# Performance work log

Hardware: AMD Instinct MI355X
Metric: run time of the kernel (lower is better)

The kernel has to match this reference:

```python
import jax, jax.numpy as jnp
import numpy as np

SEQ, B, D_IN, D_H = 512, 64, 512, 512


def setup_inputs() -> dict:
    key = jax.random.key(0)
    ks = jax.random.split(key, 5)
    s = 1.0 / np.sqrt(D_IN + D_H)
    inp = {
        "inputs": jax.random.normal(ks[0], (SEQ, B, D_IN), dtype=jnp.float32),
        "W_f": jax.random.normal(ks[1], (D_H, D_IN + D_H), dtype=jnp.float32) * s,
        "b_f": jnp.zeros((D_H,), jnp.float32),
        "W_i": jax.random.normal(ks[2], (D_H, D_IN + D_H), dtype=jnp.float32) * s,
        "b_i": jnp.zeros((D_H,), jnp.float32),
        "W_g": jax.random.normal(ks[3], (D_H, D_IN + D_H), dtype=jnp.float32) * s,
        "b_g": jnp.zeros((D_H,), jnp.float32),
        "W_o": jax.random.normal(ks[4], (D_H, D_IN + D_H), dtype=jnp.float32) * s,
        "b_o": jnp.zeros((D_H,), jnp.float32),
    }
    return inp


def reference(inputs, W_f, b_f, W_i, b_i, W_g, b_g, W_o, b_o):
    # inputs: [seq, batch, d_in]; states start at zeros (module default)
    B_ = inputs.shape[1]
    h0 = jnp.zeros((B_, D_H), inputs.dtype)
    c0 = jnp.zeros((B_, D_H), inputs.dtype)

    def step(carry, x_t):
        hx, cx = carry
        combined = jnp.concatenate([x_t, hx], axis=1)  # [B, d_in+d_h]
        f = jax.nn.sigmoid(combined @ W_f.T + b_f)
        i = jax.nn.sigmoid(combined @ W_i.T + b_i)
        g = jnp.tanh(combined @ W_g.T + b_g)
        o = jax.nn.sigmoid(combined @ W_o.T + b_o)
        cx = f * cx + i * g
        hx = o * jnp.tanh(cx)
        return (hx, cx), hx

    (hx, cx), stacked = jax.lax.scan(step, (h0, c0), inputs)
    return stacked, hx, cx
```

## Files before the change

kernel.cpp:

```cpp
#include <hip/hip_runtime.h>

#define SEQ   512
#define BATCH 64
#define DIN   512
#define DH    512
#define KTOT  1024
#define NWG   128
#define NTH   256
#define HBUF_BYTES 65536

#define FLAGS_BYTES 65536
#define HBASE_OFF   65536
#define XBF_OFF     (HBASE_OFF + 512 * HBUF_BYTES)
#define XBF_BYTES   ((size_t)SEQ * 4 * 16 * 1024)
#define WS_MODE1    ((size_t)HBASE_OFF + 511 * HBUF_BYTES)
#define WS_MODE2    ((size_t)XBF_OFF + XBF_BYTES)
#define FLAG_STRIDE 32

typedef __attribute__((ext_vector_type(8))) short short8;
typedef __attribute__((ext_vector_type(4))) float f32x4;

__device__ __forceinline__ float tanh_fast(float v) {
    const float e = __expf(2.0f * v);
    return 1.0f - 2.0f / (e + 1.0f);
}

__device__ __forceinline__ unsigned int f2bf(float f) {
    unsigned int u = __float_as_uint(f);
    return (u + 0x7fffu + ((u >> 16) & 1u)) >> 16;
}

__device__ __forceinline__ short8 cvt8(float4 lo, float4 hi) {
    short8 r;
    r[0] = (short)f2bf(lo.x); r[1] = (short)f2bf(lo.y);
    r[2] = (short)f2bf(lo.z); r[3] = (short)f2bf(lo.w);
    r[4] = (short)f2bf(hi.x); r[5] = (short)f2bf(hi.y);
    r[6] = (short)f2bf(hi.z); r[7] = (short)f2bf(hi.w);
    return r;
}

__device__ __forceinline__ unsigned int ld_flag(const unsigned int* p) {
    return __hip_atomic_load(p, __ATOMIC_RELAXED, __HIP_MEMORY_SCOPE_AGENT);
}
__device__ __forceinline__ void st_flag(unsigned int* p, unsigned int v) {
    __hip_atomic_store(p, v, __ATOMIC_RELAXED, __HIP_MEMORY_SCOPE_AGENT);
}
__device__ __forceinline__ unsigned long long ld_h_sc1(const unsigned long long* p) {
    return __hip_atomic_load(p, __ATOMIC_RELAXED, __HIP_MEMORY_SCOPE_AGENT);
}
__device__ __forceinline__ void st_h(unsigned long long* p, unsigned long long v) {
    __hip_atomic_store(p, v, __ATOMIC_RELAXED, __HIP_MEMORY_SCOPE_AGENT);
}

__global__ __launch_bounds__(256)
void xconv(const float* __restrict__ x, unsigned short* __restrict__ xbf)
{
    const int gid = blockIdx.x * 256 + threadIdx.x;
    const int l   = gid & 63;
    const int kt  = (gid >> 6) & 15;
    const int mtt = (gid >> 10) & 3;
    const int t   = gid >> 12;
    const float* src = x + ((size_t)t * BATCH + mtt * 16 + (l & 15)) * DIN
                         + kt * 32 + (l >> 4) * 8;
    *(short8*)(xbf + (size_t)gid * 8) =
        cvt8(*(const float4*)src, *(const float4*)(src + 4));
}

template <int MODE>
__global__ __launch_bounds__(NTH, 1)
void lstm_mfma(const float* __restrict__ x,
               const unsigned short* __restrict__ xbf,
               const float* __restrict__ Wf, const float* __restrict__ bfp,
               const float* __restrict__ Wi, const float* __restrict__ bip,
               const float* __restrict__ Wg, const float* __restrict__ bgp,
               const float* __restrict__ Wo, const float* __restrict__ bop,
               float* __restrict__ out,
               unsigned int* __restrict__ ws_u32)
{
    const int tid = threadIdx.x;
    const int l   = tid & 63;
    const int mt  = tid >> 6;
    const int wg  = blockIdx.x;
    const int j0  = wg * 4;

    const int n    = l & 15;
    const int khi  = l >> 4;
    const bool isg = (khi == 2);

    unsigned int* const flags = ws_u32;
    char* const hbase = (char*)ws_u32 + HBASE_OFF;

    const float* Wn = (n < 8) ? ((n < 4) ? Wf : Wi) : ((n < 12) ? Wg : Wo);
    const float* wrow = Wn + (size_t)(j0 + (n & 3)) * KTOT + khi * 8;
    short8 Bfr[32];
    #pragma unroll
    for (int kt = 0; kt < 32; ++kt) {
        Bfr[kt] = cvt8(*(const float4*)(wrow + kt * 32),
                       *(const float4*)(wrow + kt * 32 + 4));
    }
    const float* bptr = (khi == 0) ? bfp : (khi == 1) ? bip : (khi == 2) ? bgp : bop;
    const float4 bias4 = *(const float4*)(bptr + j0);

    float cst0 = 0.f, cst1 = 0.f, cst2 = 0.f, cst3 = 0.f;

    float* const hx_out = out + (size_t)SEQ * BATCH * DH;
    float* const cx_out = hx_out + (size_t)BATCH * DH;

    const int kth         = wg >> 3;
    const int lane_f_base = ((wg & 7) >> 1) << 4;
    const int half8       = (wg & 1) * 8;

    const unsigned int* const f0p = flags + ((size_t)mt * 128 + l) * FLAG_STRIDE;
    const unsigned int* const f1p = f0p + (size_t)64 * FLAG_STRIDE;
    unsigned int* const my_flag = flags + ((size_t)mt * 128 + wg) * FLAG_STRIDE;

    const float*  xrow_base = x + (size_t)(mt * 16 + (l & 15)) * DIN + khi * 8;
    const short8* xbf_base  = (const short8*)xbf + (size_t)mt * 16 * 64 + l;

    for (int t = 0; t < SEQ; ++t) {
        f32x4 acc_a = {0.f, 0.f, 0.f, 0.f};
        f32x4 acc_b = {0.f, 0.f, 0.f, 0.f};

        if (MODE == 2) {
            const short8* xp = xbf_base + (size_t)t * 4096;
            #pragma unroll
            for (int kt = 0; kt < 16; kt += 2) {
                acc_a = __builtin_amdgcn_mfma_f32_16x16x32_bf16(Bfr[kt], xp[kt * 64],
                                                                acc_a, 0, 0, 0);
                acc_b = __builtin_amdgcn_mfma_f32_16x16x32_bf16(Bfr[kt + 1], xp[(kt + 1) * 64],
                                                                acc_b, 0, 0, 0);
            }
        } else {
            const float* xr = xrow_base + (size_t)t * BATCH * DIN;
            #pragma unroll
            for (int kt = 0; kt < 16; kt += 2) {
                const short8 a0 = cvt8(*(const float4*)(xr + kt * 32),
                                       *(const float4*)(xr + kt * 32 + 4));
                const short8 a1 = cvt8(*(const float4*)(xr + (kt + 1) * 32),
                                       *(const float4*)(xr + (kt + 1) * 32 + 4));
                acc_a = __builtin_amdgcn_mfma_f32_16x16x32_bf16(Bfr[kt], a0, acc_a, 0, 0, 0);
                acc_b = __builtin_amdgcn_mfma_f32_16x16x32_bf16(Bfr[kt + 1], a1, acc_b, 0, 0, 0);
            }
        }

        if (t > 0) {
            const unsigned int target = (unsigned int)t;
            for (;;) {
                const unsigned int fa = ld_flag(f0p);
                const unsigned int fb = ld_flag(f1p);
                if (__all(fa >= target && fb >= target)) break;
                __builtin_amdgcn_s_sleep(1);
            }
            asm volatile("" ::: "memory");

            if (MODE == 0) {
                const unsigned long long* hp =
                    (const unsigned long long*)(hbase + ((t & 1) ^ 1) * HBUF_BYTES)
                    + ((size_t)(mt * 16) * 64 + l) * 2;
                #pragma unroll
                for (int kt = 0; kt < 16; kt += 2) {
                    union { unsigned long long u[2]; short8 v; } U0, U1;
                    U0.u[0] = ld_h_sc1(hp + kt * 128);
                    U0.u[1] = ld_h_sc1(hp + kt * 128 + 1);
                    U1.u[0] = ld_h_sc1(hp + (kt + 1) * 128);
                    U1.u[1] = ld_h_sc1(hp + (kt + 1) * 128 + 1);
                    acc_a = __builtin_amdgcn_mfma_f32_16x16x32_bf16(Bfr[16 + kt], U0.v,
                                                                    acc_a, 0, 0, 0);
                    acc_b = __builtin_amdgcn_mfma_f32_16x16x32_bf16(Bfr[17 + kt], U1.v,
                                                                    acc_b, 0, 0, 0);
                }
            } else {
                const uint4* hp = (const uint4*)(hbase + (size_t)(t - 1) * HBUF_BYTES)
                                  + ((size_t)(mt * 16) * 64 + l);
                uint4 hv[16];
                #pragma unroll
                for (int kt = 0; kt < 16; ++kt) hv[kt] = hp[kt * 64];
                #pragma unroll
                for (int kt = 0; kt < 16; kt += 2) {
                    union { uint4 u; short8 v; } U0, U1;
                    U0.u = hv[kt]; U1.u = hv[kt + 1];
                    acc_a = __builtin_amdgcn_mfma_f32_16x16x32_bf16(Bfr[16 + kt], U0.v,
                                                                    acc_a, 0, 0, 0);
                    acc_b = __builtin_amdgcn_mfma_f32_16x16x32_bf16(Bfr[17 + kt], U1.v,
                                                                    acc_b, 0, 0, 0);
                }
            }
        }

        float aq0, aq1, aq2, aq3;
        {
            const float m = isg ? 2.0f : 1.0f;
            const float p0 = acc_a[0] + acc_b[0] + bias4.x;
            const float p1 = acc_a[1] + acc_b[1] + bias4.y;
            const float p2 = acc_a[2] + acc_b[2] + bias4.z;
            const float p3 = acc_a[3] + acc_b[3] + bias4.w;
            const float y0 = 1.0f / (1.0f + __expf(-m * p0));
            const float y1 = 1.0f / (1.0f + __expf(-m * p1));
            const float y2 = 1.0f / (1.0f + __expf(-m * p2));
            const float y3 = 1.0f / (1.0f + __expf(-m * p3));
            aq0 = isg ? 2.0f * y0 - 1.0f : y0;
            aq1 = isg ? 2.0f * y1 - 1.0f : y1;
            aq2 = isg ? 2.0f * y2 - 1.0f : y2;
            aq3 = isg ? 2.0f * y3 - 1.0f : y3;
        }
        const float i0 = __shfl_xor(aq0, 16), g0 = __shfl_xor(aq0, 32), o0 = __shfl_xor(aq0, 48);
        const float i1 = __shfl_xor(aq1, 16), g1 = __shfl_xor(aq1, 32), o1 = __shfl_xor(aq1, 48);
        const float i2 = __shfl_xor(aq2, 16), g2 = __shfl_xor(aq2, 32), o2 = __shfl_xor(aq2, 48);
        const float i3 = __shfl_xor(aq3, 16), g3 = __shfl_xor(aq3, 32), o3 = __shfl_xor(aq3, 48);

        const bool active = (l < 16);
        float hq0 = 0.f, hq1 = 0.f, hq2 = 0.f, hq3 = 0.f;

        if (active) {
            cst0 = fmaf(aq0, cst0, i0 * g0); hq0 = o0 * tanh_fast(cst0);
            cst1 = fmaf(aq1, cst1, i1 * g1); hq1 = o1 * tanh_fast(cst1);
            cst2 = fmaf(aq2, cst2, i2 * g2); hq2 = o2 * tanh_fast(cst2);
            cst3 = fmaf(aq3, cst3, i3 * g3); hq3 = o3 * tanh_fast(cst3);

            if (t < SEQ - 1) {
                const unsigned long long pk =
                    (unsigned long long)(f2bf(hq0) | (f2bf(hq1) << 16))
                    | ((unsigned long long)(f2bf(hq2) | (f2bf(hq3) << 16)) << 32);
                char* const wb = (MODE == 0) ? hbase + (t & 1) * HBUF_BYTES
                                             : hbase + (size_t)t * HBUF_BYTES;
                unsigned long long* hp_w = (unsigned long long*)
                    (wb + (((size_t)(mt * 16 + kth) * 64
                            + (lane_f_base | l)) << 4) + half8);
                st_h(hp_w, pk);
            }
        }

        if (t < SEQ - 1) {
            asm volatile("s_waitcnt vmcnt(0)" ::: "memory");
            if (l == 0) st_flag(my_flag, (unsigned int)(t + 1));
        }

        if (active) {
            const int b = mt * 16 + l;
            const float4 ov = make_float4(hq0, hq1, hq2, hq3);
            *(float4*)(out + ((size_t)t * BATCH + b) * DH + j0) = ov;
            if (t == SEQ - 1) {
                *(float4*)(hx_out + (size_t)b * DH + j0) = ov;
                *(float4*)(cx_out + (size_t)b * DH + j0) =
                    make_float4(cst0, cst1, cst2, cst3);
            }
        }
    }
}

extern "C" void kernel_launch(void* const* d_in, const int* in_sizes, int n_in,
                              void* d_out, int out_size, void* d_ws, size_t ws_size,
                              hipStream_t stream)
{
    const float* x  = (const float*)d_in[0];
    const float* Wf = (const float*)d_in[1];
    const float* bf = (const float*)d_in[2];
    const float* Wi = (const float*)d_in[3];
    const float* bi = (const float*)d_in[4];
    const float* Wg = (const float*)d_in[5];
    const float* bg = (const float*)d_in[6];
    const float* Wo = (const float*)d_in[7];
    const float* bo = (const float*)d_in[8];
    float* out = (float*)d_out;

    hipMemsetAsync(d_ws, 0, FLAGS_BYTES, stream);

    unsigned int* wsp = (unsigned int*)d_ws;
    if (ws_size >= WS_MODE2) {
        unsigned short* xbf = (unsigned short*)((char*)d_ws + XBF_OFF);
        xconv<<<SEQ * 4 * 16 * 64 / 256, 256, 0, stream>>>(x, xbf);
        lstm_mfma<2><<<NWG, NTH, 0, stream>>>(x, xbf, Wf, bf, Wi, bi,
                                              Wg, bg, Wo, bo, out, wsp);
    } else if (ws_size >= WS_MODE1) {
        lstm_mfma<1><<<NWG, NTH, 0, stream>>>(x, nullptr, Wf, bf, Wi, bi,
                                              Wg, bg, Wo, bo, out, wsp);
    } else {
        lstm_mfma<0><<<NWG, NTH, 0, stream>>>(x, nullptr, Wf, bf, Wi, bi,
                                              Wg, bg, Wo, bo, out, wsp);
    }
}
```

Measured before the change: 2.221 ms.

## Replace flag-based step sync with epoch-tagged hidden-state packets polled directly

Removes the separate per-workgroup flag array and the store-wait-flag sequence. Each producer now writes its hidden-state slice as a 16-byte packet that carries an epoch tag next to the data, and consumers spin on the data loads until every tag matches the expected step. This takes one global round trip (flag write, flag poll, then data load) off the serial recurrence critical path. It also drops the bf16 x-preconversion kernel and the workspace memset, so x is converted inline again. In exchange it doubles the hidden-state traffic, relies on 16-byte stores being seen atomically, and adds a bounded-spin bailout.

```diff
diff --git a/kernel.cpp b/kernel.cpp
--- a/kernel.cpp
+++ b/kernel.cpp
@@ -7,29 +7,22 @@
 #define KTOT  1024
 #define NWG   128
 #define NTH   256
-#define HBUF_BYTES 65536
-
-#define FLAGS_BYTES 65536
-#define HBASE_OFF   65536
-#define XBF_OFF     (HBASE_OFF + 512 * HBUF_BYTES)
-#define XBF_BYTES   ((size_t)SEQ * 4 * 16 * 1024)
-#define WS_MODE1    ((size_t)HBASE_OFF + 511 * HBUF_BYTES)
-#define WS_MODE2    ((size_t)XBF_OFF + XBF_BYTES)
-#define FLAG_STRIDE 32
+#define SLABBYTES 131072
+#define EPMAGIC 0x5A5A0000u
+#define SWEEP_BOUND 262144u
 
 typedef __attribute__((ext_vector_type(8))) short short8;
 typedef __attribute__((ext_vector_type(4))) float f32x4;
+typedef __attribute__((ext_vector_type(4))) unsigned int u32x4;
 
 __device__ __forceinline__ float tanh_fast(float v) {
     const float e = __expf(2.0f * v);
     return 1.0f - 2.0f / (e + 1.0f);
 }
-
 __device__ __forceinline__ unsigned int f2bf(float f) {
     unsigned int u = __float_as_uint(f);
     return (u + 0x7fffu + ((u >> 16) & 1u)) >> 16;
 }
-
 __device__ __forceinline__ short8 cvt8(float4 lo, float4 hi) {
     short8 r;
     r[0] = (short)f2bf(lo.x); r[1] = (short)f2bf(lo.y);
@@ -39,43 +32,14 @@
     return r;
 }
 
-__device__ __forceinline__ unsigned int ld_flag(const unsigned int* p) {
-    return __hip_atomic_load(p, __ATOMIC_RELAXED, __HIP_MEMORY_SCOPE_AGENT);
-}
-__device__ __forceinline__ void st_flag(unsigned int* p, unsigned int v) {
-    __hip_atomic_store(p, v, __ATOMIC_RELAXED, __HIP_MEMORY_SCOPE_AGENT);
-}
-__device__ __forceinline__ unsigned long long ld_h_sc1(const unsigned long long* p) {
-    return __hip_atomic_load(p, __ATOMIC_RELAXED, __HIP_MEMORY_SCOPE_AGENT);
-}
-__device__ __forceinline__ void st_h(unsigned long long* p, unsigned long long v) {
-    __hip_atomic_store(p, v, __ATOMIC_RELAXED, __HIP_MEMORY_SCOPE_AGENT);
-}
-
-__global__ __launch_bounds__(256)
-void xconv(const float* __restrict__ x, unsigned short* __restrict__ xbf)
-{
-    const int gid = blockIdx.x * 256 + threadIdx.x;
-    const int l   = gid & 63;
-    const int kt  = (gid >> 6) & 15;
-    const int mtt = (gid >> 10) & 3;
-    const int t   = gid >> 12;
-    const float* src = x + ((size_t)t * BATCH + mtt * 16 + (l & 15)) * DIN
-                         + kt * 32 + (l >> 4) * 8;
-    *(short8*)(xbf + (size_t)gid * 8) =
-        cvt8(*(const float4*)src, *(const float4*)(src + 4));
-}
-
-template <int MODE>
 __global__ __launch_bounds__(NTH, 1)
 void lstm_mfma(const float* __restrict__ x,
-               const unsigned short* __restrict__ xbf,
                const float* __restrict__ Wf, const float* __restrict__ bfp,
                const float* __restrict__ Wi, const float* __restrict__ bip,
                const float* __restrict__ Wg, const float* __restrict__ bgp,
                const float* __restrict__ Wo, const float* __restrict__ bop,
                float* __restrict__ out,
-               unsigned int* __restrict__ ws_u32)
+               char* __restrict__ slab)
 {
     const int tid = threadIdx.x;
     const int l   = tid & 63;
@@ -86,9 +50,6 @@
     const int n    = l & 15;
     const int khi  = l >> 4;
     const bool isg = (khi == 2);
-
-    unsigned int* const flags = ws_u32;
-    char* const hbase = (char*)ws_u32 + HBASE_OFF;
 
     const float* Wn = (n < 8) ? ((n < 4) ? Wf : Wi) : ((n < 12) ? Wg : Wo);
     const float* wrow = Wn + (size_t)(j0 + (n & 3)) * KTOT + khi * 8;
@@ -102,35 +63,24 @@
     const float4 bias4 = *(const float4*)(bptr + j0);
 
     float cst0 = 0.f, cst1 = 0.f, cst2 = 0.f, cst3 = 0.f;
-
     float* const hx_out = out + (size_t)SEQ * BATCH * DH;
     float* const cx_out = hx_out + (size_t)BATCH * DH;
 
     const int kth         = wg >> 3;
     const int lane_f_base = ((wg & 7) >> 1) << 4;
-    const int half8       = (wg & 1) * 8;
-
-    const unsigned int* const f0p = flags + ((size_t)mt * 128 + l) * FLAG_STRIDE;
-    const unsigned int* const f1p = f0p + (size_t)64 * FLAG_STRIDE;
-    unsigned int* const my_flag = flags + ((size_t)mt * 128 + wg) * FLAG_STRIDE;
-
-    const float*  xrow_base = x + (size_t)(mt * 16 + (l & 15)) * DIN + khi * 8;
-    const short8* xbf_base  = (const short8*)xbf + (size_t)mt * 16 * 64 + l;
-
-    for (int t = 0; t < SEQ; ++t) {
+    const size_t prod_off = ((((size_t)(mt * 16 + kth) * 64)
+                             + (size_t)(lane_f_base | l)) << 5)
+                          + (size_t)(wg & 1) * 16;
+
+    const float* xrow_base = x + (size_t)(mt * 16 + n) * DIN + khi * 8;
+
+    bool dead = false;
+
+    for (int t = 0; t < SEQ && !dead; ++t) {
         f32x4 acc_a = {0.f, 0.f, 0.f, 0.f};
         f32x4 acc_b = {0.f, 0.f, 0.f, 0.f};
 
-        if (MODE == 2) {
-            const short8* xp = xbf_base + (size_t)t * 4096;
-            #pragma unroll
-            for (int kt = 0; kt < 16; kt += 2) {
-                acc_a = __builtin_amdgcn_mfma_f32_16x16x32_bf16(Bfr[kt], xp[kt * 64],
-                                                                acc_a, 0, 0, 0);
-                acc_b = __builtin_amdgcn_mfma_f32_16x16x32_bf16(Bfr[kt + 1], xp[(kt + 1) * 64],
-                                                                acc_b, 0, 0, 0);
-            }
-        } else {
+        {
             const float* xr = xrow_base + (size_t)t * BATCH * DIN;
             #pragma unroll
             for (int kt = 0; kt < 16; kt += 2) {
@@ -144,47 +94,77 @@
         }
 
         if (t > 0) {
-            const unsigned int target = (unsigned int)t;
-            for (;;) {
-                const unsigned int fa = ld_flag(f0p);
-                const unsigned int fb = ld_flag(f1p);
-                if (__all(fa >= target && fb >= target)) break;
-                __builtin_amdgcn_s_sleep(1);
-            }
-            asm volatile("" ::: "memory");
-
-            if (MODE == 0) {
-                const unsigned long long* hp =
-                    (const unsigned long long*)(hbase + ((t & 1) ^ 1) * HBUF_BYTES)
-                    + ((size_t)(mt * 16) * 64 + l) * 2;
-                #pragma unroll
-                for (int kt = 0; kt < 16; kt += 2) {
-                    union { unsigned long long u[2]; short8 v; } U0, U1;
-                    U0.u[0] = ld_h_sc1(hp + kt * 128);
-                    U0.u[1] = ld_h_sc1(hp + kt * 128 + 1);
-                    U1.u[0] = ld_h_sc1(hp + (kt + 1) * 128);
-                    U1.u[1] = ld_h_sc1(hp + (kt + 1) * 128 + 1);
-                    acc_a = __builtin_amdgcn_mfma_f32_16x16x32_bf16(Bfr[16 + kt], U0.v,
-                                                                    acc_a, 0, 0, 0);
-                    acc_b = __builtin_amdgcn_mfma_f32_16x16x32_bf16(Bfr[17 + kt], U1.v,
-                                                                    acc_b, 0, 0, 0);
+            const unsigned int e = EPMAGIC | (unsigned int)(t - 1);
+            const char* hb = slab + (size_t)((t & 1) ^ 1) * SLABBYTES
+                           + (((size_t)(mt * 16) * 64 + l) << 5);
+
+            #pragma unroll
+            for (int hf = 0; hf < 2; ++hf) {
+                const char* b0 = hb + hf * 16384;
+                const char* b1 = b0 + 4096;
+                const char* b2 = b0 + 8192;
+                const char* b3 = b0 + 12288;
+                u32x4 q0, q1, q2, q3, q4, q5, q6, q7;
+                u32x4 q8, q9, qA, qB, qC, qD, qE, qF;
+                for (unsigned int it = 0;; ++it) {
+                    asm volatile(
+                        "global_load_dwordx4 %0,  %16, off sc0 sc1\n\t"
+                        "global_load_dwordx4 %1,  %16, off offset:16 sc0 sc1\n\t"
+                        "global_load_dwordx4 %2,  %16, off offset:2048 sc0 sc1\n\t"
+                        "global_load_dwordx4 %3,  %16, off offset:2064 sc0 sc1\n\t"
+                        "global_load_dwordx4 %4,  %17, off sc0 sc1\n\t"
+                        "global_load_dwordx4 %5,  %17, off offset:16 sc0 sc1\n\t"
+                        "global_load_dwordx4 %6,  %17, off offset:2048 sc0 sc1\n\t"
+                        "global_load_dwordx4 %7,  %17, off offset:2064 sc0 sc1\n\t"
+                        "global_load_dwordx4 %8,  %18, off sc0 sc1\n\t"
+                        "global_load_dwordx4 %9,  %18, off offset:16 sc0 sc1\n\t"
+                        "global_load_dwordx4 %10, %18, off offset:2048 sc0 sc1\n\t"
+                        "global_load_dwordx4 %11, %18, off offset:2064 sc0 sc1\n\t"
+                        "global_load_dwordx4 %12, %19, off sc0 sc1\n\t"
+                        "global_load_dwordx4 %13, %19, off offset:16 sc0 sc1\n\t"
+                        "global_load_dwordx4 %14, %19, off offset:2048 sc0 sc1\n\t"
+                        "global_load_dwordx4 %15, %19, off offset:2064 sc0 sc1\n\t"
+                        "s_waitcnt vmcnt(0)"
+                        : "=&v"(q0), "=&v"(q1), "=&v"(q2), "=&v"(q3),
+                          "=&v"(q4), "=&v"(q5), "=&v"(q6), "=&v"(q7),
+                          "=&v"(q8), "=&v"(q9), "=&v"(qA), "=&v"(qB),
+                          "=&v"(qC), "=&v"(qD), "=&v"(qE), "=&v"(qF)
+                        : "v"(b0), "v"(b1), "v"(b2), "v"(b3)
+                        : "memory");
+                    const unsigned int bad =
+                        (q0[1]^e)|(q0[3]^e)|(q1[1]^e)|(q1[3]^e)|
+                        (q2[1]^e)|(q2[3]^e)|(q3[1]^e)|(q3[3]^e)|
+                        (q4[1]^e)|(q4[3]^e)|(q5[1]^e)|(q5[3]^e)|
+                        (q6[1]^e)|(q6[3]^e)|(q7[1]^e)|(q7[3]^e)|
+                        (q8[1]^e)|(q8[3]^e)|(q9[1]^e)|(q9[3]^e)|
+                        (qA[1]^e)|(qA[3]^e)|(qB[1]^e)|(qB[3]^e)|
+                        (qC[1]^e)|(qC[3]^e)|(qD[1]^e)|(qD[3]^e)|
+                        (qE[1]^e)|(qE[3]^e)|(qF[1]^e)|(qF[3]^e);
+                    if (__all(bad == 0u)) break;
+                    if (it >= SWEEP_BOUND) { dead = true; break; }
+                    __builtin_amdgcn_s_sleep(1);
                 }
-            } else {
-                const uint4* hp = (const uint4*)(hbase + (size_t)(t - 1) * HBUF_BYTES)
-                                  + ((size_t)(mt * 16) * 64 + l);
-                uint4 hv[16];
-                #pragma unroll
-                for (int kt = 0; kt < 16; ++kt) hv[kt] = hp[kt * 64];
-                #pragma unroll
-                for (int kt = 0; kt < 16; kt += 2) {
-                    union { uint4 u; short8 v; } U0, U1;
-                    U0.u = hv[kt]; U1.u = hv[kt + 1];
-                    acc_a = __builtin_amdgcn_mfma_f32_16x16x32_bf16(Bfr[16 + kt], U0.v,
-                                                                    acc_a, 0, 0, 0);
-                    acc_b = __builtin_amdgcn_mfma_f32_16x16x32_bf16(Bfr[17 + kt], U1.v,
-                                                                    acc_b, 0, 0, 0);
+                if (dead) break;
+
+#define DOKT(KT, QA, QB) { u32x4 fv; fv[0] = QA[0]; fv[1] = QA[2];            \
+    fv[2] = QB[0]; fv[3] = QB[2];                                             \
+    union { u32x4 u; short8 v; } Uu; Uu.u = fv;                               \
+    if ((KT) & 1) acc_b = __builtin_amdgcn_mfma_f32_16x16x32_bf16(            \
+                              Bfr[16 + (KT)], Uu.v, acc_b, 0, 0, 0);          \
+    else          acc_a = __builtin_amdgcn_mfma_f32_16x16x32_bf16(            \
+                              Bfr[16 + (KT)], Uu.v, acc_a, 0, 0, 0); }
+                if (hf == 0) {
+                    DOKT(0, q0, q1)  DOKT(1, q2, q3)  DOKT(2, q4, q5)
+                    DOKT(3, q6, q7)  DOKT(4, q8, q9)  DOKT(5, qA, qB)
+                    DOKT(6, qC, qD)  DOKT(7, qE, qF)
+                } else {
+                    DOKT(8, q0, q1)  DOKT(9, q2, q3)  DOKT(10, q4, q5)
+                    DOKT(11, q6, q7) DOKT(12, q8, q9) DOKT(13, qA, qB)
+                    DOKT(14, qC, qD) DOKT(15, qE, qF)
                 }
-            }
+#undef DOKT
+            }
+            if (dead) break;
         }
 
         float aq0, aq1, aq2, aq3;
@@ -218,24 +198,16 @@
             cst3 = fmaf(aq3, cst3, i3 * g3); hq3 = o3 * tanh_fast(cst3);
 
             if (t < SEQ - 1) {
-                const unsigned long long pk =
-                    (unsigned long long)(f2bf(hq0) | (f2bf(hq1) << 16))
-                    | ((unsigned long long)(f2bf(hq2) | (f2bf(hq3) << 16)) << 32);
-                char* const wb = (MODE == 0) ? hbase + (t & 1) * HBUF_BYTES
-                                             : hbase + (size_t)t * HBUF_BYTES;
-                unsigned long long* hp_w = (unsigned long long*)
-                    (wb + (((size_t)(mt * 16 + kth) * 64
-                            + (lane_f_base | l)) << 4) + half8);
-                st_h(hp_w, pk);
-            }
-        }
-
-        if (t < SEQ - 1) {
-            asm volatile("s_waitcnt vmcnt(0)" ::: "memory");
-            if (l == 0) st_flag(my_flag, (unsigned int)(t + 1));
-        }
-
-        if (active) {
+                u32x4 pkt;
+                pkt[0] = f2bf(hq0) | (f2bf(hq1) << 16);
+                pkt[1] = EPMAGIC | (unsigned int)t;
+                pkt[2] = f2bf(hq2) | (f2bf(hq3) << 16);
+                pkt[3] = EPMAGIC | (unsigned int)t;
+                char* hp_w = slab + (size_t)(t & 1) * SLABBYTES + prod_off;
+                asm volatile("global_store_dwordx4 %0, %1, off sc0 sc1"
+                             :: "v"(hp_w), "v"(pkt) : "memory");
+            }
+
             const int b = mt * 16 + l;
             const float4 ov = make_float4(hq0, hq1, hq2, hq3);
             *(float4*)(out + ((size_t)t * BATCH + b) * DH + j0) = ov;
@@ -263,19 +235,6 @@
     const float* bo = (const float*)d_in[8];
     float* out = (float*)d_out;
 
-    hipMemsetAsync(d_ws, 0, FLAGS_BYTES, stream);
-
-    unsigned int* wsp = (unsigned int*)d_ws;
-    if (ws_size >= WS_MODE2) {
-        unsigned short* xbf = (unsigned short*)((char*)d_ws + XBF_OFF);
-        xconv<<<SEQ * 4 * 16 * 64 / 256, 256, 0, stream>>>(x, xbf);
-        lstm_mfma<2><<<NWG, NTH, 0, stream>>>(x, xbf, Wf, bf, Wi, bi,
-                                              Wg, bg, Wo, bo, out, wsp);
-    } else if (ws_size >= WS_MODE1) {
-        lstm_mfma<1><<<NWG, NTH, 0, stream>>>(x, nullptr, Wf, bf, Wi, bi,
-                                              Wg, bg, Wo, bo, out, wsp);
-    } else {
-        lstm_mfma<0><<<NWG, NTH, 0, stream>>>(x, nullptr, Wf, bf, Wi, bi,
-                                              Wg, bg, Wo, bo, out, wsp);
-    }
-}
+    lstm_mfma<<<NWG, NTH, 0, stream>>>(x, Wf, bf, Wi, bi, Wg, bg, Wo, bo,
+                                       out, (char*)d_ws);
+}
```

New measurement: 2.966 ms. 1.34x slower.
